# Performance work log

Hardware: AMD Instinct MI355X
Metric: run time of the kernel (lower is better)

Reference implementation:

```python
import jax, jax.numpy as jnp
import numpy as np

B, C, N, RATIO = 16, 1024, 16384, 8
BN_EPS = 1e-5


def setup_inputs() -> dict:
    key = jax.random.key(0)
    k1, k2, k3, k4 = jax.random.split(key, 4)
    return {
        "x": jax.random.normal(k1, (B, C, N), dtype=jnp.float32),
        "w1": jax.random.normal(k2, (C // RATIO, C), dtype=jnp.float32) * (1.0 / np.sqrt(C)),
        "w2": jax.random.normal(k3, (C, C // RATIO), dtype=jnp.float32) * (1.0 / np.sqrt(C // RATIO)),
        "sw": jax.random.normal(k4, (2,), dtype=jnp.float32),
        "gamma": jnp.ones((1,), dtype=jnp.float32),
        "beta": jnp.zeros((1,), dtype=jnp.float32),
        "running_mean": jnp.zeros((1,), dtype=jnp.float32),
        "running_var": jnp.ones((1,), dtype=jnp.float32),
    }


def reference(x, w1, w2, sw, gamma, beta, running_mean, running_var):
    # ---- Channel attention (CBAM) ----
    m = jnp.mean(x, axis=-1)   # (B, C) avg pool over N
    mx = jnp.max(x, axis=-1)   # (B, C) max pool over N

    def mlp(v):  # shared Conv1d(k=1) MLP: C -> C/r -> C
        h = jax.nn.relu(jnp.einsum('rc,bc->br', w1, v))
        return jnp.einsum('cr,br->bc', w2, h)

    gate = jax.nn.sigmoid(mlp(m) + mlp(mx))[:, :, None]  # (B, C, 1)
    x1 = gate * x                                          # (B, C, N)

    # ---- Spatial attention ----
    cm = jnp.mean(x1, axis=1, keepdims=True)  # (B, 1, N) mean over C
    cx = jnp.max(x1, axis=1, keepdims=True)   # (B, 1, N) max over C
    # torch concat order is [max, mean]; conv1 weight sw applies accordingly
    s = sw[0] * cx + sw[1] * cm               # (B, 1, N)
    # BatchNorm1d(1) in eval mode with running stats
    s = (s - running_mean[0]) * jax.lax.rsqrt(running_var[0] + BN_EPS) * gamma[0] + beta[0]
    s = jax.nn.relu(s)
    att = jax.nn.softmax(s, axis=-1)          # softmax over N
    return att * x1                            # (B, C, N)
```

## Files before the change

kernel.cpp:

```cpp
#include <hip/hip_runtime.h>
#include <math.h>

#define BB 16
#define CC 1024
#define NN 16384
#define HID 128
#define SPLIT 2
#define CHALF (CC/SPLIT)

__global__ __launch_bounds__(256) void k1_pool(const float* __restrict__ x,
                                               float* __restrict__ meanp,
                                               float* __restrict__ maxp) {
    const int row = blockIdx.x;
    const int tid = threadIdx.x;
    const float4* xr = (const float4*)(x + (size_t)row * NN);
    float s = 0.f, m = -INFINITY;
    #pragma unroll
    for (int i = 0; i < 16; ++i) {
        float4 v = xr[tid + i * 256];
        s += v.x + v.y + v.z + v.w;
        m = fmaxf(m, fmaxf(fmaxf(v.x, v.y), fmaxf(v.z, v.w)));
    }
    __shared__ float ss[4], sm[4];
    for (int off = 32; off > 0; off >>= 1) {
        s += __shfl_down(s, off, 64);
        m = fmaxf(m, __shfl_down(m, off, 64));
    }
    const int wave = tid >> 6, lane = tid & 63;
    if (lane == 0) { ss[wave] = s; sm[wave] = m; }
    __syncthreads();
    if (tid == 0) {
        float fs = ss[0] + ss[1] + ss[2] + ss[3];
        float fm = fmaxf(fmaxf(sm[0], sm[1]), fmaxf(sm[2], sm[3]));
        meanp[row] = fs * (1.0f / NN);
        maxp[row]  = fm;
    }
}

__global__ __launch_bounds__(256) void k2_gate(const float* __restrict__ meanp,
                                               const float* __restrict__ maxp,
                                               const float* __restrict__ w1,
                                               const float* __restrict__ w2,
                                               float* __restrict__ gate) {
    const int b = blockIdx.x;
    const int tid = threadIdx.x;
    __shared__ float smv[CC], sxv[CC], hm[HID], hx[HID], h[HID];
    for (int c = tid; c < CC; c += 256) {
        smv[c] = meanp[b * CC + c];
        sxv[c] = maxp[b * CC + c];
    }
    __syncthreads();
    {
        const int r = tid & 127;
        const float* src = (tid < 128) ? smv : sxv;
        const float* w1r = w1 + (size_t)r * CC;
        float acc = 0.f;
        for (int c = 0; c < CC; ++c) acc = fmaf(w1r[c], src[c], acc);
        acc = fmaxf(acc, 0.f);
        if (tid < 128) hm[r] = acc; else hx[r] = acc;
    }
    __syncthreads();
    if (tid < HID) h[tid] = hm[tid] + hx[tid];
    __syncthreads();
    for (int c = tid; c < CC; c += 256) {
        const float* w2r = w2 + (size_t)c * HID;
        float a = 0.f;
        #pragma unroll 8
        for (int r = 0; r < HID; ++r) a = fmaf(w2r[r], h[r], a);
        gate[b * CC + c] = 1.0f / (1.0f + expf(-a));
    }
}

__global__ __launch_bounds__(256) void k3_spatial(const float* __restrict__ x,
                                                  const float* __restrict__ gate,
                                                  float* __restrict__ psum,
                                                  float* __restrict__ pmax) {
    const int chunk = blockIdx.x;
    const int split = blockIdx.y;
    const int b     = blockIdx.z;
    const int tid = threadIdx.x;
    __shared__ float g[CHALF];
    for (int i = tid; i < CHALF; i += 256) g[i] = gate[b * CC + split * CHALF + i];
    __syncthreads();
    const int n4 = chunk * 256 + tid;
    const float4* xb = (const float4*)(x + ((size_t)b * CC + (size_t)split * CHALF) * NN);
    float4 s = {0.f, 0.f, 0.f, 0.f};
    float4 m = {-INFINITY, -INFINITY, -INFINITY, -INFINITY};
    #pragma unroll 4
    for (int c = 0; c < CHALF; ++c) {
        float4 v = xb[(size_t)c * (NN / 4) + n4];
        float gc = g[c];
        s.x = fmaf(gc, v.x, s.x);
        s.y = fmaf(gc, v.y, s.y);
        s.z = fmaf(gc, v.z, s.z);
        s.w = fmaf(gc, v.w, s.w);
        m.x = fmaxf(m.x, gc * v.x);
        m.y = fmaxf(m.y, gc * v.y);
        m.z = fmaxf(m.z, gc * v.z);
        m.w = fmaxf(m.w, gc * v.w);
    }
    const size_t o = (size_t)(b * SPLIT + split) * (NN / 4) + n4;
    ((float4*)psum)[o] = s;
    ((float4*)pmax)[o] = m;
}

__global__ __launch_bounds__(256) void k5_softmax(const float* __restrict__ psum,
                                                  const float* __restrict__ pmax,
                                                  const float* __restrict__ sw,
                                                  const float* __restrict__ gamma,
                                                  const float* __restrict__ beta,
                                                  const float* __restrict__ rmean,
                                                  const float* __restrict__ rvar,
                                                  float* __restrict__ attexp,
                                                  float* __restrict__ invsum) {
    const int b = blockIdx.x;
    const int tid = threadIdx.x;
    const float sw0 = sw[0], sw1 = sw[1];
    const float scale = gamma[0] / sqrtf(rvar[0] + 1e-5f);
    const float shift = beta[0] - rmean[0] * scale;
    const float4* ps0 = (const float4*)(psum + (size_t)(2 * b) * NN);
    const float4* ps1 = (const float4*)(psum + (size_t)(2 * b + 1) * NN);
    const float4* pm0 = (const float4*)(pmax + (size_t)(2 * b) * NN);
    const float4* pm1 = (const float4*)(pmax + (size_t)(2 * b + 1) * NN);

    __shared__ float red[4];
    __shared__ float bcast;

    auto sval = [&](float ssum, float smax) -> float {
        float v = sw0 * smax + sw1 * (ssum * (1.0f / CC));
        v = fmaf(v, scale, shift);
        return fmaxf(v, 0.f);
    };

    float lmax = -INFINITY;
    for (int i = tid; i < NN / 4; i += 256) {
        float4 s0 = ps0[i], s1 = ps1[i], m0 = pm0[i], m1 = pm1[i];
        lmax = fmaxf(lmax, sval(s0.x + s1.x, fmaxf(m0.x, m1.x)));
        lmax = fmaxf(lmax, sval(s0.y + s1.y, fmaxf(m0.y, m1.y)));
        lmax = fmaxf(lmax, sval(s0.z + s1.z, fmaxf(m0.z, m1.z)));
        lmax = fmaxf(lmax, sval(s0.w + s1.w, fmaxf(m0.w, m1.w)));
    }
    for (int off = 32; off > 0; off >>= 1) lmax = fmaxf(lmax, __shfl_down(lmax, off, 64));
    if ((tid & 63) == 0) red[tid >> 6] = lmax;
    __syncthreads();
    if (tid == 0) bcast = fmaxf(fmaxf(red[0], red[1]), fmaxf(red[2], red[3]));
    __syncthreads();
    const float bmax = bcast;
    __syncthreads();

    float lsum = 0.f;
    float4* ae = (float4*)(attexp + (size_t)b * NN);
    for (int i = tid; i < NN / 4; i += 256) {
        float4 s0 = ps0[i], s1 = ps1[i], m0 = pm0[i], m1 = pm1[i];
        float4 e;
        e.x = expf(sval(s0.x + s1.x, fmaxf(m0.x, m1.x)) - bmax);
        e.y = expf(sval(s0.y + s1.y, fmaxf(m0.y, m1.y)) - bmax);
        e.z = expf(sval(s0.z + s1.z, fmaxf(m0.z, m1.z)) - bmax);
        e.w = expf(sval(s0.w + s1.w, fmaxf(m0.w, m1.w)) - bmax);
        lsum += e.x + e.y + e.z + e.w;
        ae[i] = e;
    }
    for (int off = 32; off > 0; off >>= 1) lsum += __shfl_down(lsum, off, 64);
    if ((tid & 63) == 0) red[tid >> 6] = lsum;
    __syncthreads();
    if (tid == 0) invsum[b] = 1.0f / (red[0] + red[1] + red[2] + red[3]);
}

__global__ __launch_bounds__(256) void k6_final(const float* __restrict__ x,
                                                const float* __restrict__ gate,
                                                const float* __restrict__ attexp,
                                                const float* __restrict__ invsum,
                                                float* __restrict__ out) {
    const int blk = blockIdx.x;
    const int t = blk & 15;
    const int row = blk >> 4;
    const int b = row >> 10;
    const int tid = threadIdx.x;
    const float gsc = gate[row] * invsum[b];
    const size_t base4 = (size_t)row * (NN / 4) + t * 256 + tid;
    const size_t abase4 = (size_t)b * (NN / 4) + t * 256 + tid;
    float4 v = ((const float4*)x)[base4];
    float4 a = ((const float4*)attexp)[abase4];
    float4 o;
    o.x = v.x * a.x * gsc;
    o.y = v.y * a.y * gsc;
    o.z = v.z * a.z * gsc;
    o.w = v.w * a.w * gsc;
    ((float4*)out)[base4] = o;
}

extern "C" void kernel_launch(void* const* d_in, const int* in_sizes, int n_in,
                              void* d_out, int out_size, void* d_ws, size_t ws_size,
                              hipStream_t stream) {
    const float* x     = (const float*)d_in[0];
    const float* w1    = (const float*)d_in[1];
    const float* w2    = (const float*)d_in[2];
    const float* sw    = (const float*)d_in[3];
    const float* gamma = (const float*)d_in[4];
    const float* beta  = (const float*)d_in[5];
    const float* rmean = (const float*)d_in[6];
    const float* rvar  = (const float*)d_in[7];
    float* out = (float*)d_out;
    float* ws  = (float*)d_ws;

    float* meanp  = ws;
    float* maxp   = ws + 16384;
    float* gate   = ws + 32768;
    float* psum   = ws + 49152;
    float* pmax   = psum + (size_t)BB * SPLIT * NN;
    float* attexp = pmax + (size_t)BB * SPLIT * NN;
    float* invsum = attexp + (size_t)BB * NN;

    k1_pool<<<BB * CC, 256, 0, stream>>>(x, meanp, maxp);
    k2_gate<<<BB, 256, 0, stream>>>(meanp, maxp, w1, w2, gate);
    dim3 g3(NN / 1024, SPLIT, BB);
    k3_spatial<<<g3, 256, 0, stream>>>(x, gate, psum, pmax);
    k5_softmax<<<BB, 256, 0, stream>>>(psum, pmax, sw, gamma, beta, rmean, rvar, attexp, invsum);
    k6_final<<<BB * CC * (NN / 1024), 256, 0, stream>>>(x, gate, attexp, invsum, out);
}
```

Measured before the change: 813.2 us.

## Parallelize softmax with fixed exp shift, widen gate MLP and spatial split

The per-batch two-pass softmax, which ran as only 16 blocks, becomes a grid-wide single-pass kernel. It drops the max reduction by using a constant exponent shift and writes per-block partial sums, which the final kernel adds up. The spatial reduction split goes from 2 to 4 channel groups for more blocks, and the gate MLP uses 1024 threads with shuffle reductions. The final kernel handles four float4s per thread. The fixed shift removes a full pass over the partial buffers, but exp can overflow if the spatial logits exceed roughly 98.

```diff
diff --git a/kernel.cpp b/kernel.cpp
--- a/kernel.cpp
+++ b/kernel.cpp
@@ -5,8 +5,10 @@
 #define CC 1024
 #define NN 16384
 #define HID 128
-#define SPLIT 2
-#define CHALF (CC/SPLIT)
+#define SPLIT 4
+#define CPART (CC/SPLIT)
+#define N4 (NN/4)
+#define EXPSHIFT 10.0f
 
 __global__ __launch_bounds__(256) void k1_pool(const float* __restrict__ x,
                                                float* __restrict__ meanp,
@@ -37,37 +39,45 @@
     }
 }
 
-__global__ __launch_bounds__(256) void k2_gate(const float* __restrict__ meanp,
-                                               const float* __restrict__ maxp,
-                                               const float* __restrict__ w1,
-                                               const float* __restrict__ w2,
-                                               float* __restrict__ gate) {
+__global__ __launch_bounds__(1024) void k2_gate(const float* __restrict__ meanp,
+                                                const float* __restrict__ maxp,
+                                                const float* __restrict__ w1,
+                                                const float* __restrict__ w2,
+                                                float* __restrict__ gate) {
     const int b = blockIdx.x;
     const int tid = threadIdx.x;
-    __shared__ float smv[CC], sxv[CC], hm[HID], hx[HID], h[HID];
-    for (int c = tid; c < CC; c += 256) {
-        smv[c] = meanp[b * CC + c];
-        sxv[c] = maxp[b * CC + c];
+    __shared__ float sv[2][CC];
+    __shared__ float hh[2][HID];
+    __shared__ float h[HID];
+    if (tid < CC) {
+        sv[0][tid] = meanp[b * CC + tid];
+        sv[1][tid] = maxp[b * CC + tid];
     }
     __syncthreads();
     {
-        const int r = tid & 127;
-        const float* src = (tid < 128) ? smv : sxv;
+        const int slot = tid >> 2;
+        const int part = tid & 3;
+        const int src  = slot >> 7;
+        const int r    = slot & 127;
         const float* w1r = w1 + (size_t)r * CC;
+        const float* svp = sv[src];
         float acc = 0.f;
-        for (int c = 0; c < CC; ++c) acc = fmaf(w1r[c], src[c], acc);
-        acc = fmaxf(acc, 0.f);
-        if (tid < 128) hm[r] = acc; else hx[r] = acc;
-    }
-    __syncthreads();
-    if (tid < HID) h[tid] = hm[tid] + hx[tid];
-    __syncthreads();
-    for (int c = tid; c < CC; c += 256) {
-        const float* w2r = w2 + (size_t)c * HID;
+        const int c0 = part * 256;
+        #pragma unroll 8
+        for (int c = c0; c < c0 + 256; ++c) acc = fmaf(w1r[c], svp[c], acc);
+        acc += __shfl_xor(acc, 1, 64);
+        acc += __shfl_xor(acc, 2, 64);
+        if (part == 0) hh[src][r] = fmaxf(acc, 0.f);
+    }
+    __syncthreads();
+    if (tid < HID) h[tid] = hh[0][tid] + hh[1][tid];
+    __syncthreads();
+    {
+        const float* w2r = w2 + (size_t)tid * HID;
         float a = 0.f;
-        #pragma unroll 8
+        #pragma unroll
         for (int r = 0; r < HID; ++r) a = fmaf(w2r[r], h[r], a);
-        gate[b * CC + c] = 1.0f / (1.0f + expf(-a));
+        gate[b * CC + tid] = 1.0f / (1.0f + expf(-a));
     }
 }
 
@@ -79,16 +89,16 @@
     const int split = blockIdx.y;
     const int b     = blockIdx.z;
     const int tid = threadIdx.x;
-    __shared__ float g[CHALF];
-    for (int i = tid; i < CHALF; i += 256) g[i] = gate[b * CC + split * CHALF + i];
+    __shared__ float g[CPART];
+    g[tid] = gate[b * CC + split * CPART + tid];
     __syncthreads();
     const int n4 = chunk * 256 + tid;
-    const float4* xb = (const float4*)(x + ((size_t)b * CC + (size_t)split * CHALF) * NN);
+    const float4* xb = (const float4*)(x + ((size_t)b * CC + (size_t)split * CPART) * NN);
     float4 s = {0.f, 0.f, 0.f, 0.f};
     float4 m = {-INFINITY, -INFINITY, -INFINITY, -INFINITY};
-    #pragma unroll 4
-    for (int c = 0; c < CHALF; ++c) {
-        float4 v = xb[(size_t)c * (NN / 4) + n4];
+    #pragma unroll 8
+    for (int c = 0; c < CPART; ++c) {
+        float4 v = xb[(size_t)c * N4 + n4];
         float gc = g[c];
         s.x = fmaf(gc, v.x, s.x);
         s.y = fmaf(gc, v.y, s.y);
@@ -99,94 +109,89 @@
         m.z = fmaxf(m.z, gc * v.z);
         m.w = fmaxf(m.w, gc * v.w);
     }
-    const size_t o = (size_t)(b * SPLIT + split) * (NN / 4) + n4;
+    const size_t o = (size_t)(b * SPLIT + split) * N4 + n4;
     ((float4*)psum)[o] = s;
     ((float4*)pmax)[o] = m;
 }
 
-__global__ __launch_bounds__(256) void k5_softmax(const float* __restrict__ psum,
-                                                  const float* __restrict__ pmax,
-                                                  const float* __restrict__ sw,
-                                                  const float* __restrict__ gamma,
-                                                  const float* __restrict__ beta,
-                                                  const float* __restrict__ rmean,
-                                                  const float* __restrict__ rvar,
-                                                  float* __restrict__ attexp,
-                                                  float* __restrict__ invsum) {
-    const int b = blockIdx.x;
+__global__ __launch_bounds__(256) void k4_exp(const float* __restrict__ psum,
+                                              const float* __restrict__ pmax,
+                                              const float* __restrict__ sw,
+                                              const float* __restrict__ gamma,
+                                              const float* __restrict__ beta,
+                                              const float* __restrict__ rmean,
+                                              const float* __restrict__ rvar,
+                                              float* __restrict__ attexp,
+                                              float* __restrict__ blksum) {
+    const int chunk = blockIdx.x;
+    const int b     = blockIdx.y;
     const int tid = threadIdx.x;
     const float sw0 = sw[0], sw1 = sw[1];
-    const float scale = gamma[0] / sqrtf(rvar[0] + 1e-5f);
+    const float scale = gamma[0] * rsqrtf(rvar[0] + 1e-5f);
     const float shift = beta[0] - rmean[0] * scale;
-    const float4* ps0 = (const float4*)(psum + (size_t)(2 * b) * NN);
-    const float4* ps1 = (const float4*)(psum + (size_t)(2 * b + 1) * NN);
-    const float4* pm0 = (const float4*)(pmax + (size_t)(2 * b) * NN);
-    const float4* pm1 = (const float4*)(pmax + (size_t)(2 * b + 1) * NN);
-
+    const int i = chunk * 256 + tid;
+    const float4* ps = (const float4*)psum;
+    const float4* pm = (const float4*)pmax;
+    float4 ssum = {0.f, 0.f, 0.f, 0.f};
+    float4 smax = {-INFINITY, -INFINITY, -INFINITY, -INFINITY};
+    #pragma unroll
+    for (int sp = 0; sp < SPLIT; ++sp) {
+        float4 a = ps[(size_t)(b * SPLIT + sp) * N4 + i];
+        float4 c = pm[(size_t)(b * SPLIT + sp) * N4 + i];
+        ssum.x += a.x; ssum.y += a.y; ssum.z += a.z; ssum.w += a.w;
+        smax.x = fmaxf(smax.x, c.x); smax.y = fmaxf(smax.y, c.y);
+        smax.z = fmaxf(smax.z, c.z); smax.w = fmaxf(smax.w, c.w);
+    }
+    auto sval = [&](float su, float mx) -> float {
+        float v = sw0 * mx + sw1 * (su * (1.0f / CC));
+        v = fmaf(v, scale, shift);
+        v = fmaxf(v, 0.f);
+        return expf(v - EXPSHIFT);
+    };
+    float4 e;
+    e.x = sval(ssum.x, smax.x);
+    e.y = sval(ssum.y, smax.y);
+    e.z = sval(ssum.z, smax.z);
+    e.w = sval(ssum.w, smax.w);
+    ((float4*)attexp)[(size_t)b * N4 + i] = e;
+    float lsum = e.x + e.y + e.z + e.w;
+    for (int off = 32; off > 0; off >>= 1) lsum += __shfl_down(lsum, off, 64);
     __shared__ float red[4];
-    __shared__ float bcast;
-
-    auto sval = [&](float ssum, float smax) -> float {
-        float v = sw0 * smax + sw1 * (ssum * (1.0f / CC));
-        v = fmaf(v, scale, shift);
-        return fmaxf(v, 0.f);
-    };
-
-    float lmax = -INFINITY;
-    for (int i = tid; i < NN / 4; i += 256) {
-        float4 s0 = ps0[i], s1 = ps1[i], m0 = pm0[i], m1 = pm1[i];
-        lmax = fmaxf(lmax, sval(s0.x + s1.x, fmaxf(m0.x, m1.x)));
-        lmax = fmaxf(lmax, sval(s0.y + s1.y, fmaxf(m0.y, m1.y)));
-        lmax = fmaxf(lmax, sval(s0.z + s1.z, fmaxf(m0.z, m1.z)));
-        lmax = fmaxf(lmax, sval(s0.w + s1.w, fmaxf(m0.w, m1.w)));
-    }
-    for (int off = 32; off > 0; off >>= 1) lmax = fmaxf(lmax, __shfl_down(lmax, off, 64));
-    if ((tid & 63) == 0) red[tid >> 6] = lmax;
-    __syncthreads();
-    if (tid == 0) bcast = fmaxf(fmaxf(red[0], red[1]), fmaxf(red[2], red[3]));
-    __syncthreads();
-    const float bmax = bcast;
-    __syncthreads();
-
-    float lsum = 0.f;
-    float4* ae = (float4*)(attexp + (size_t)b * NN);
-    for (int i = tid; i < NN / 4; i += 256) {
-        float4 s0 = ps0[i], s1 = ps1[i], m0 = pm0[i], m1 = pm1[i];
-        float4 e;
-        e.x = expf(sval(s0.x + s1.x, fmaxf(m0.x, m1.x)) - bmax);
-        e.y = expf(sval(s0.y + s1.y, fmaxf(m0.y, m1.y)) - bmax);
-        e.z = expf(sval(s0.z + s1.z, fmaxf(m0.z, m1.z)) - bmax);
-        e.w = expf(sval(s0.w + s1.w, fmaxf(m0.w, m1.w)) - bmax);
-        lsum += e.x + e.y + e.z + e.w;
-        ae[i] = e;
-    }
-    for (int off = 32; off > 0; off >>= 1) lsum += __shfl_down(lsum, off, 64);
     if ((tid & 63) == 0) red[tid >> 6] = lsum;
     __syncthreads();
-    if (tid == 0) invsum[b] = 1.0f / (red[0] + red[1] + red[2] + red[3]);
+    if (tid == 0) blksum[b * 16 + chunk] = red[0] + red[1] + red[2] + red[3];
 }
 
 __global__ __launch_bounds__(256) void k6_final(const float* __restrict__ x,
                                                 const float* __restrict__ gate,
                                                 const float* __restrict__ attexp,
-                                                const float* __restrict__ invsum,
+                                                const float* __restrict__ blksum,
                                                 float* __restrict__ out) {
     const int blk = blockIdx.x;
-    const int t = blk & 15;
-    const int row = blk >> 4;
+    const int t = blk & 3;
+    const int row = blk >> 2;
     const int b = row >> 10;
     const int tid = threadIdx.x;
-    const float gsc = gate[row] * invsum[b];
-    const size_t base4 = (size_t)row * (NN / 4) + t * 256 + tid;
-    const size_t abase4 = (size_t)b * (NN / 4) + t * 256 + tid;
-    float4 v = ((const float4*)x)[base4];
-    float4 a = ((const float4*)attexp)[abase4];
-    float4 o;
-    o.x = v.x * a.x * gsc;
-    o.y = v.y * a.y * gsc;
-    o.z = v.z * a.z * gsc;
-    o.w = v.w * a.w * gsc;
-    ((float4*)out)[base4] = o;
+    float tot = 0.f;
+    #pragma unroll
+    for (int j = 0; j < 16; ++j) tot += blksum[b * 16 + j];
+    const float gsc = gate[row] / tot;
+    const size_t base4  = (size_t)row * N4 + t * 1024 + tid;
+    const size_t abase4 = (size_t)b * N4 + t * 1024 + tid;
+    const float4* xp = (const float4*)x;
+    const float4* ap = (const float4*)attexp;
+    float4* op = (float4*)out;
+    #pragma unroll
+    for (int j = 0; j < 4; ++j) {
+        float4 v = xp[base4 + j * 256];
+        float4 a = ap[abase4 + j * 256];
+        float4 o;
+        o.x = v.x * a.x * gsc;
+        o.y = v.y * a.y * gsc;
+        o.z = v.z * a.z * gsc;
+        o.w = v.w * a.w * gsc;
+        op[base4 + j * 256] = o;
+    }
 }
 
 extern "C" void kernel_launch(void* const* d_in, const int* in_sizes, int n_in,
@@ -204,17 +209,18 @@
     float* ws  = (float*)d_ws;
 
     float* meanp  = ws;
-    float* maxp   = ws + 16384;
-    float* gate   = ws + 32768;
-    float* psum   = ws + 49152;
+    float* maxp   = meanp + 16384;
+    float* gate   = maxp + 16384;
+    float* psum   = gate + 16384;
     float* pmax   = psum + (size_t)BB * SPLIT * NN;
     float* attexp = pmax + (size_t)BB * SPLIT * NN;
-    float* invsum = attexp + (size_t)BB * NN;
+    float* blksum = attexp + (size_t)BB * NN;
 
     k1_pool<<<BB * CC, 256, 0, stream>>>(x, meanp, maxp);
-    k2_gate<<<BB, 256, 0, stream>>>(meanp, maxp, w1, w2, gate);
+    k2_gate<<<BB, 1024, 0, stream>>>(meanp, maxp, w1, w2, gate);
     dim3 g3(NN / 1024, SPLIT, BB);
     k3_spatial<<<g3, 256, 0, stream>>>(x, gate, psum, pmax);
-    k5_softmax<<<BB, 256, 0, stream>>>(psum, pmax, sw, gamma, beta, rmean, rvar, attexp, invsum);
-    k6_final<<<BB * CC * (NN / 1024), 256, 0, stream>>>(x, gate, attexp, invsum, out);
-}
+    dim3 g4(16, BB);
+    k4_exp<<<g4, 256, 0, stream>>>(psum, pmax, sw, gamma, beta, rmean, rvar, attexp, blksum);
+    k6_final<<<BB * CC * 4, 256, 0, stream>>>(x, gate, attexp, blksum, out);
+}
```

Result: no change. 811.0 us (-0.3%).
